# Kernel optimization log

Measured on AMD Instinct MI355X. Metric: run time of the kernel, lower is better.

## Reference

```python
import jax, jax.numpy as jnp
import numpy as np

B = 4
C = 128           # input channels
H = W = 512       # image size
P = 16            # patch size
GH = GW = 32      # token grid (H//P, W//P)
N = GH * GW       # num patches = 1024
PATCH_DIM = C * P * P  # 32768
DIM = 512         # embed dim
MLP = 256         # ffn hidden
DH = 64           # dim per head
HEADS = (2, 4, 8) # per-layer head counts
NUM_REL = (2 * GH - 1) * (2 * GW - 1)  # 3969


def _rel_index():
    # faithful to the torch buffer construction (meshgrid default 'ij')
    coords = np.stack(np.meshgrid(np.arange(GH), np.arange(GW), indexing='ij')).reshape(2, -1)
    rc = (coords[:, :, None] - coords[:, None, :]).transpose(1, 2, 0)  # [N,N,2]
    rc[..., 0] += GH - 1
    rc[..., 1] += GW - 1
    rc[..., 0] *= 2 * GH - 1
    return jnp.asarray(rc.sum(-1))  # [N,N] int

REL_IDX = _rel_index()


def _ln(x, s, b):
    m = x.mean(-1, keepdims=True)
    v = x.var(-1, keepdims=True)
    return (x - m) / jnp.sqrt(v + 1e-5) * s + b


def setup_inputs() -> dict:
    key = jax.random.key(0)
    ks = iter(jax.random.split(key, 40))
    def rn(shape, scale=0.02):
        return jax.random.normal(next(ks), shape, jnp.float32) * scale
    inp = {"img": jax.random.normal(next(ks), (B, C, H, W), jnp.float32)}
    inp["patch_w"] = rn((PATCH_DIM, DIM))
    inp["patch_b"] = jnp.zeros((DIM,), jnp.float32)
    inp["pos_emb"] = rn((1, N, DIM), 1.0)
    inp["ln1_s"] = jnp.ones((3, DIM), jnp.float32)
    inp["ln1_b"] = jnp.zeros((3, DIM), jnp.float32)
    inp["ln2_s"] = jnp.ones((3, DIM), jnp.float32)
    inp["ln2_b"] = jnp.zeros((3, DIM), jnp.float32)
    for l, h in enumerate(HEADS):
        inner = DH * h
        inp[f"qkv_w{l}"] = rn((DIM, 3 * inner))
        inp[f"out_w{l}"] = rn((inner, DIM))
        inp[f"out_b{l}"] = jnp.zeros((DIM,), jnp.float32)
        inp[f"bias{l}"] = rn((NUM_REL, h))
    inp["ff_w1"] = rn((3, DIM, MLP))
    inp["ff_b1"] = jnp.zeros((3, MLP), jnp.float32)
    inp["ff_w2"] = rn((3, MLP, DIM))
    inp["ff_b2"] = jnp.zeros((3, DIM), jnp.float32)
    return inp


def reference(img, patch_w, patch_b, pos_emb, ln1_s, ln1_b, ln2_s, ln2_b,
              qkv_w0, qkv_w1, qkv_w2, out_w0, out_w1, out_w2,
              out_b0, out_b1, out_b2, bias0, bias1, bias2,
              ff_w1, ff_b1, ff_w2, ff_b2):
    b = img.shape[0]
    # Rearrange 'b c (h p1) (w p2) -> b (h w) (p1 p2 c)'
    x = img.reshape(b, C, GH, P, GW, P).transpose(0, 2, 4, 3, 5, 1).reshape(b, N, PATCH_DIM)
    x = x @ patch_w + patch_b + pos_emb

    qkv_ws = (qkv_w0, qkv_w1, qkv_w2)
    out_ws = (out_w0, out_w1, out_w2)
    out_bs = (out_b0, out_b1, out_b2)
    tables = (bias0, bias1, bias2)

    for l, h in enumerate(HEADS):
        # attention with relative position bias
        xn = _ln(x, ln1_s[l], ln1_b[l])
        qkv = xn @ qkv_ws[l]                                  # [b, N, 3*h*DH]
        q, k, v = jnp.split(qkv, 3, axis=-1)
        q = q.reshape(b, N, h, DH).transpose(0, 2, 1, 3)      # bhnd
        k = k.reshape(b, N, h, DH).transpose(0, 2, 1, 3)
        v = v.reshape(b, N, h, DH).transpose(0, 2, 1, 3)
        dots = jnp.einsum('bhnd,bhmd->bhnm', q, k) * (DH ** -0.5)
        rel = tables[l][REL_IDX].transpose(2, 0, 1)           # [h, N, N]
        attn = jax.nn.softmax(dots + rel[None], axis=-1)
        o = jnp.einsum('bhnm,bhmd->bhnd', attn, v)
        o = o.transpose(0, 2, 1, 3).reshape(b, N, h * DH)
        x = o @ out_ws[l] + out_bs[l] + x
        # feed-forward
        xn = _ln(x, ln2_s[l], ln2_b[l])
        hmid = jax.nn.gelu(xn @ ff_w1[l] + ff_b1[l], approximate=False)
        x = hmid @ ff_w2[l] + ff_b2[l] + x

    return x.transpose(0, 2, 1).reshape(b, DIM, GH, GW)
```

## Files before the change

kernel.cpp:

```cpp
#include <hip/hip_runtime.h>

typedef unsigned short u16;
typedef __bf16 bf16x8 __attribute__((ext_vector_type(8)));
typedef float f32x4 __attribute__((ext_vector_type(4)));

#define AS1 __attribute__((address_space(1)))
#define AS3 __attribute__((address_space(3)))
#define MFMA(a,b,c) __builtin_amdgcn_mfma_f32_16x16x32_bf16(a,b,c,0,0,0)

__device__ __forceinline__ u16 f2bf(float f) {
    union { float f; unsigned u; } x; x.f = f;
    unsigned r = x.u + 0x7fffu + ((x.u >> 16) & 1u);
    return (u16)(r >> 16);
}

__global__ void k_patch_wT(const float* __restrict__ w, u16* __restrict__ o)
{
    __shared__ u16 T[256*33];
    int c = blockIdx.x, n0 = blockIdx.y*32;
    int t = threadIdx.x;
    int rr = t >> 5, cc = t & 31;
    #pragma unroll
    for (int i = 0; i < 32; ++i) {
        int r = i*8 + rr;
        int k = (r >> 4)*2048 + (r & 15)*128 + c;
        T[r*33 + cc] = f2bf(w[(size_t)k*512 + n0 + cc]);
    }
    __syncthreads();
    #pragma unroll
    for (int i = 0; i < 4; ++i) {
        int j  = i*8 + (t >> 5);
        int ch = t & 31;
        union { u16 u[8]; uint4 v; } pk;
        #pragma unroll
        for (int q = 0; q < 8; ++q) pk.u[q] = T[(ch*8+q)*33 + j];
        *(uint4*)(o + (size_t)(n0 + j)*32768 + c*256 + ch*8) = pk.v;
    }
}

__global__ void k_init_x(float* __restrict__ x, const float* __restrict__ pb, const float* __restrict__ pe)
{
    int i4 = blockIdx.x*256 + threadIdx.x;
    size_t base = (size_t)i4*4;
    float4 a = *(const float4*)(pb + (base & 511));
    float4 b = *(const float4*)(pe + (base & 524287));
    float4 r = make_float4(a.x+b.x, a.y+b.y, a.z+b.z, a.w+b.w);
    *(float4*)(x + base) = r;
}

struct TXJob { const float* in; u16* out; int K, N, tiles; };
struct TXArgs { TXJob j[12]; };

__global__ void k_wT_all(TXArgs a)
{
    __shared__ float T[32*33];
    int bid = blockIdx.x;
    int ji = 0;
    while (bid >= a.j[ji].tiles) { bid -= a.j[ji].tiles; ++ji; }
    const float* __restrict__ in = a.j[ji].in;
    u16* __restrict__ o = a.j[ji].out;
    const int K = a.j[ji].K, N = a.j[ji].N;
    const int tn = N >> 5;
    const int kt = (bid / tn) * 32, nt = (bid % tn) * 32;
    int t = threadIdx.x, r = t >> 5, c = t & 31;
    #pragma unroll
    for (int i = 0; i < 4; ++i)
        T[(r + i*8)*33 + c] = in[(size_t)(kt + r + i*8)*N + nt + c];
    __syncthreads();
    #pragma unroll
    for (int i = 0; i < 4; ++i)
        o[(size_t)(nt + r + i*8)*K + kt + c] = f2bf(T[c*33 + r + i*8]);
}

__global__ __launch_bounds__(1024) void k_patch_gemm(
    const float* __restrict__ img, const u16* __restrict__ Bt, float* __restrict__ Cf)
{
    __shared__ alignas(16) u16 As[2*128*64];
    __shared__ alignas(16) u16 Bs[2*512*64];
    const int t = threadIdx.x;
    const int bid = blockIdx.x;
    const int z = bid & 7;
    const int tile = bid >> 3;
    const int b = tile >> 3, gh0 = (tile & 7)*4;
    const int m0 = tile*128;
    const int wave = t >> 6, lane = t & 63;
    const int r16 = lane & 15, g = lane >> 4;
    const int wm = (wave >> 3)*64, wn = (wave & 7)*64;

    const int arow = t >> 6;
    const int ghl = arow >> 2, p1l = arow & 3;
    const int aw = (t & 63)*8;
    const int tok = ghl*32 + (aw >> 4);
    unsigned abyte = (unsigned)(tok*128 + p1l*32 + (aw & 15)*2);
    abyte ^= (unsigned)((tok & 7) << 4);
    const float* imgb = img + (size_t)b*128*262144
                      + (size_t)((gh0 + ghl)*16 + p1l)*512 + aw;
    const int brow = t >> 3;
    const int bchunk = (t & 7) ^ (brow & 7);
    const u16* Bb = Bt + (size_t)brow*32768 + (size_t)z*4096 + bchunk*8;
    u16* Bsd = Bs + t*8;

    f32x4 acc[4][4];
    const f32x4 zz = {0.f,0.f,0.f,0.f};
    #pragma unroll
    for (int im = 0; im < 4; ++im)
        #pragma unroll
        for (int in_ = 0; in_ < 4; ++in_) acc[im][in_] = zz;

#define ALOAD(KC) do {                                                               \
    const int c_ = z*16 + ((KC) >> 2);                                               \
    const float* s_ = imgb + (size_t)c_*262144 + ((KC) & 3)*2048;                    \
    e0 = *(const float4*)s_;  e1 = *(const float4*)(s_ + 4); } while(0)
#define AWRITE(BUF) do {                                                             \
    union { u16 u[8]; uint4 v; } pk_;                                                \
    pk_.u[0]=f2bf(e0.x); pk_.u[1]=f2bf(e0.y); pk_.u[2]=f2bf(e0.z); pk_.u[3]=f2bf(e0.w); \
    pk_.u[4]=f2bf(e1.x); pk_.u[5]=f2bf(e1.y); pk_.u[6]=f2bf(e1.z); pk_.u[7]=f2bf(e1.w); \
    *(uint4*)((char*)As + (BUF)*16384 + abyte) = pk_.v; } while(0)
#define BSTAGE(KC, BUF) do { _Pragma("unroll")                                       \
    for (int i_ = 0; i_ < 4; ++i_)                                                   \
        __builtin_amdgcn_global_load_lds((AS1 void*)(Bb + (size_t)i_*128*32768 + (KC)*64), \
                                         (AS3 void*)(Bsd + (BUF)*32768 + i_*8192), 16, 0, 0); } while(0)
#define WAITVM(N) asm volatile("s_waitcnt vmcnt(" #N ")" ::: "memory")
#define WAITLG   asm volatile("s_waitcnt lgkmcnt(0)" ::: "memory")

    float4 e0, e1;
    ALOAD(0);
    BSTAGE(0, 0);
    WAITVM(4);
    AWRITE(0);
    ALOAD(1);
    BSTAGE(1, 1);
    WAITLG;
    WAITVM(6);
    __builtin_amdgcn_s_barrier();
    __builtin_amdgcn_sched_barrier(0);

    int cur = 0;
    for (int kc = 0; kc < 64; ++kc) {
        const char* Asb = (const char*)As + cur*16384;
        const char* Bsb = (const char*)Bs + cur*65536;
        #pragma unroll
        for (int kk = 0; kk < 64; kk += 32) {
            bf16x8 af[4], bfr[4];
            #pragma unroll
            for (int im = 0; im < 4; ++im) {
                unsigned off = ((unsigned)((wm + im*16 + r16)*128 + kk*2 + g*16))
                             ^ (unsigned)((r16 & 7) << 4);
                af[im] = *(const bf16x8*)(Asb + off);
            }
            #pragma unroll
            for (int in_ = 0; in_ < 4; ++in_) {
                unsigned off = ((unsigned)((wn + in_*16 + r16)*128 + kk*2 + g*16))
                             ^ (unsigned)((r16 & 7) << 4);
                bfr[in_] = *(const bf16x8*)(Bsb + off);
            }
            #pragma unroll
            for (int im = 0; im < 4; ++im)
                #pragma unroll
                for (int in_ = 0; in_ < 4; ++in_)
                    acc[im][in_] = MFMA(af[im], bfr[in_], acc[im][in_]);
        }
        if (kc < 63) {
            WAITVM(4);
            AWRITE(cur ^ 1);
        }
        WAITLG;
        __builtin_amdgcn_s_barrier();
        if (kc < 62) {
            ALOAD(kc + 2);
            BSTAGE(kc + 2, cur);
            WAITVM(6);
        } else {
            WAITVM(0);
        }
        __builtin_amdgcn_sched_barrier(0);
        cur ^= 1;
    }
#undef ALOAD
#undef AWRITE
#undef BSTAGE
#undef WAITVM
#undef WAITLG
    #pragma unroll
    for (int im = 0; im < 4; ++im) {
        int row = m0 + wm + im*16 + g*4;
        #pragma unroll
        for (int in_ = 0; in_ < 4; ++in_) {
            int col = wn + in_*16 + r16;
            #pragma unroll
            for (int r = 0; r < 4; ++r)
                __hip_atomic_fetch_add(&Cf[(size_t)(row + r)*512 + col], acc[im][in_][r],
                                       __ATOMIC_RELAXED, __HIP_MEMORY_SCOPE_AGENT);
        }
    }
}

__global__ void k_ln(const float* __restrict__ x, const float* __restrict__ sc,
                     const float* __restrict__ bi, u16* __restrict__ o)
{
    int row = blockIdx.x, lane = threadIdx.x;
    const float* xr = x + (size_t)row*512 + lane*8;
    float4 v0 = *(const float4*)xr;
    float4 v1 = *(const float4*)(xr + 4);
    float vv[8] = {v0.x,v0.y,v0.z,v0.w,v1.x,v1.y,v1.z,v1.w};
    float sum = 0.f, sq = 0.f;
    #pragma unroll
    for (int i = 0; i < 8; ++i) { sum += vv[i]; sq += vv[i]*vv[i]; }
    #pragma unroll
    for (int m = 1; m < 64; m <<= 1) { sum += __shfl_xor(sum, m, 64); sq += __shfl_xor(sq, m, 64); }
    float mean = sum * (1.f/512.f);
    float var  = sq  * (1.f/512.f) - mean*mean;
    float rstd = rsqrtf(var + 1e-5f);
    int d = lane*8;
    union { u16 u[8]; uint4 v; } pk;
    #pragma unroll
    for (int i = 0; i < 8; ++i) pk.u[i] = f2bf((vv[i]-mean)*rstd*sc[d+i] + bi[d+i]);
    *(uint4*)(o + (size_t)row*512 + d) = pk.v;
}

template<int EPI, int KB>
__global__ __launch_bounds__(256) void k_gemm(
    const u16* __restrict__ A, int lda,
    const u16* __restrict__ Bt, int ldb,
    float* __restrict__ Cf, u16* __restrict__ Cb, int ldc,
    const float* __restrict__ bias)
{
    __shared__ alignas(16) u16 As[128*64];
    __shared__ alignas(16) u16 Bs[128*64];
    const int t = threadIdx.x;
    const int m0 = blockIdx.x*128, n0 = blockIdx.y*128;
    const int wave = t >> 6, lane = t & 63;
    const int wm = (wave >> 1)*64, wn = (wave & 1)*64;
    const int r16 = lane & 15, g = lane >> 4;
    const u16* Ab = A + (size_t)(m0 + (t>>3))*lda + (t&7)*8;
    const u16* Bb = Bt + (size_t)(n0 + (t>>3))*ldb + (t&7)*8;
    u16* Asd = As + t*8;
    u16* Bsd = Bs + t*8;
    f32x4 acc[4][4];
    const f32x4 z4 = {0.f,0.f,0.f,0.f};
    #pragma unroll
    for (int im = 0; im < 4; ++im)
        #pragma unroll
        for (int in_ = 0; in_ < 4; ++in_) acc[im][in_] = z4;

    #pragma unroll
    for (int k = 0; k < KB; k += 64) {
        #pragma unroll
        for (int i = 0; i < 4; ++i) {
            __builtin_amdgcn_global_load_lds((AS1 void*)(Ab + (size_t)i*32*lda + k), (AS3 void*)(Asd + i*2048), 16, 0, 0);
            __builtin_amdgcn_global_load_lds((AS1 void*)(Bb + (size_t)i*32*ldb + k), (AS3 void*)(Bsd + i*2048), 16, 0, 0);
        }
        __syncthreads();
        #pragma unroll
        for (int kk = 0; kk < 64; kk += 32) {
            bf16x8 af[4], bfr[4];
            #pragma unroll
            for (int im = 0; im < 4; ++im)
                af[im] = *(const bf16x8*)(As + (wm + im*16 + r16)*64 + kk + g*8);
            #pragma unroll
            for (int in_ = 0; in_ < 4; ++in_)
                bfr[in_] = *(const bf16x8*)(Bs + (wn + in_*16 + r16)*64 + kk + g*8);
            #pragma unroll
            for (int im = 0; im < 4; ++im)
                #pragma unroll
                for (int in_ = 0; in_ < 4; ++in_)
                    acc[im][in_] = MFMA(af[im], bfr[in_], acc[im][in_]);
        }
        __syncthreads();
    }
    #pragma unroll
    for (int im = 0; im < 4; ++im) {
        int row = m0 + wm + im*16 + g*4;
        #pragma unroll
        for (int in_ = 0; in_ < 4; ++in_) {
            int col = n0 + wn + in_*16 + r16;
            #pragma unroll
            for (int r = 0; r < 4; ++r) {
                float v = acc[im][in_][r];
                size_t idx = (size_t)(row + r)*ldc + col;
                if constexpr (EPI == 1) {
                    Cb[idx] = f2bf(v);
                } else if constexpr (EPI == 2) {
                    float xv = v + bias[col];
                    Cb[idx] = f2bf(0.5f*xv*(1.f + erff(xv*0.70710678118654752f)));
                } else {
                    Cf[idx] += v + bias[col];
                }
            }
        }
    }
}

__global__ __launch_bounds__(256) void k_attn(
    const u16* __restrict__ qkv, const float* __restrict__ bt,
    u16* __restrict__ o, int H)
{
    const int LD = 80;
    __shared__ alignas(16) u16 Qs[64*80], Ks[64*80], Vs[64*80];
    __shared__ alignas(16) u16 Ps[4][16*80];
    const int inner = H*64, s3 = 3*inner;
    const int qt = blockIdx.x, head = blockIdx.y, b = blockIdx.z;
    const int t = threadIdx.x, wave = t >> 6, lane = t & 63;
    const int r16 = lane & 15, g = lane >> 4;
    const int q0 = qt*64;
    const size_t tokbase = (size_t)b*1024;
    const int hoff = head*64;

    #pragma unroll
    for (int it = 0; it < 2; ++it) {
        int flat = it*256 + t, r = flat >> 3, d0 = (flat & 7)*8;
        uint4 v = *(const uint4*)(qkv + (tokbase + q0 + r)*s3 + hoff + d0);
        *(uint4*)(Qs + r*LD + d0) = v;
    }
    __syncthreads();
    bf16x8 aQ0 = *(const bf16x8*)(Qs + (wave*16 + r16)*LD + g*8);
    bf16x8 aQ1 = *(const bf16x8*)(Qs + (wave*16 + r16)*LD + 32 + g*8);

    float m_[4], l_[4];
    f32x4 O[4];
    const f32x4 z4 = {0.f,0.f,0.f,0.f};
    #pragma unroll
    for (int r = 0; r < 4; ++r) { m_[r] = -1e30f; l_[r] = 0.f; O[r] = z4; }
    const int qg_base = q0 + wave*16 + g*4;

    for (int kt = 0; kt < 16; ++kt) {
        const int key0 = kt*64;
        #pragma unroll
        for (int it = 0; it < 2; ++it) {
            int flat = it*256 + t, r = flat >> 3, d0 = (flat & 7)*8;
            uint4 v = *(const uint4*)(qkv + (tokbase + key0 + r)*s3 + inner + hoff + d0);
            *(uint4*)(Ks + r*LD + d0) = v;
        }
        #pragma unroll
        for (int it = 0; it < 2; ++it) {
            int flat = it*256 + t, key = flat & 63, d0 = (flat >> 6)*8;
            uint4 v = *(const uint4*)(qkv + (tokbase + key0 + key)*s3 + 2*inner + hoff + d0);
            const u16* pv = (const u16*)&v;
            #pragma unroll
            for (int i = 0; i < 8; ++i) Vs[(d0+i)*LD + key] = pv[i];
        }
        __syncthreads();

        float Sv[4][4];
        #pragma unroll
        for (int kb = 0; kb < 4; ++kb) {
            bf16x8 k0f = *(const bf16x8*)(Ks + (kb*16 + r16)*LD + g*8);
            bf16x8 k1f = *(const bf16x8*)(Ks + (kb*16 + r16)*LD + 32 + g*8);
            f32x4 S = z4;
            S = MFMA(aQ0, k0f, S);
            S = MFMA(aQ1, k1f, S);
            int keyg = key0 + kb*16 + r16;
            int kgh = keyg >> 5, kgw = keyg & 31;
            #pragma unroll
            for (int r = 0; r < 4; ++r) {
                int qg = qg_base + r;
                int rel = ((qg >> 5) - kgh + 31)*63 + ((qg & 31) - kgw + 31);
                Sv[kb][r] = S[r]*0.125f + bt[rel*H + head];
            }
        }
        float mx[4], al[4], ps[4];
        #pragma unroll
        for (int r = 0; r < 4; ++r)
            mx[r] = fmaxf(fmaxf(Sv[0][r], Sv[1][r]), fmaxf(Sv[2][r], Sv[3][r]));
        #pragma unroll
        for (int msk = 1; msk < 16; msk <<= 1)
            #pragma unroll
            for (int r = 0; r < 4; ++r) mx[r] = fmaxf(mx[r], __shfl_xor(mx[r], msk, 64));
        #pragma unroll
        for (int r = 0; r < 4; ++r) {
            float nm = fmaxf(m_[r], mx[r]);
            al[r] = __expf(m_[r] - nm);
            m_[r] = nm;
            ps[r] = 0.f;
        }
        #pragma unroll
        for (int kb = 0; kb < 4; ++kb)
            #pragma unroll
            for (int r = 0; r < 4; ++r) {
                float p = __expf(Sv[kb][r] - m_[r]);
                Sv[kb][r] = p;
                ps[r] += p;
            }
        #pragma unroll
        for (int msk = 1; msk < 16; msk <<= 1)
            #pragma unroll
            for (int r = 0; r < 4; ++r) ps[r] += __shfl_xor(ps[r], msk, 64);
        #pragma unroll
        for (int r = 0; r < 4; ++r) l_[r] = l_[r]*al[r] + ps[r];
        #pragma unroll
        for (int kb = 0; kb < 4; ++kb)
            #pragma unroll
            for (int r = 0; r < 4; ++r)
                Ps[wave][(g*4 + r)*LD + kb*16 + r16] = f2bf(Sv[kb][r]);
        #pragma unroll
        for (int dt = 0; dt < 4; ++dt)
            #pragma unroll
            for (int r = 0; r < 4; ++r) O[dt][r] = O[dt][r]*al[r];
        __syncthreads();
        bf16x8 aP0 = *(const bf16x8*)(Ps[wave] + r16*LD + g*8);
        bf16x8 aP1 = *(const bf16x8*)(Ps[wave] + r16*LD + 32 + g*8);
        #pragma unroll
        for (int dt = 0; dt < 4; ++dt) {
            bf16x8 v0 = *(const bf16x8*)(Vs + (dt*16 + r16)*LD + g*8);
            bf16x8 v1 = *(const bf16x8*)(Vs + (dt*16 + r16)*LD + 32 + g*8);
            O[dt] = MFMA(aP0, v0, O[dt]);
            O[dt] = MFMA(aP1, v1, O[dt]);
        }
        __syncthreads();
    }
    #pragma unroll
    for (int dt = 0; dt < 4; ++dt)
        #pragma unroll
        for (int r = 0; r < 4; ++r) {
            int token = q0 + wave*16 + g*4 + r;
            o[(tokbase + token)*inner + hoff + dt*16 + r16] = f2bf(O[dt][r] / l_[r]);
        }
}

__global__ void k_out_transpose(const float* __restrict__ x, float* __restrict__ o)
{
    __shared__ float T[32*33];
    int d0 = blockIdx.x*32, n0 = blockIdx.y*32, b = blockIdx.z;
    int t = threadIdx.x, r = t >> 5, c = t & 31;
    #pragma unroll
    for (int i = 0; i < 4; ++i)
        T[(r+i*8)*33 + c] = x[((size_t)b*1024 + n0 + r + i*8)*512 + d0 + c];
    __syncthreads();
    #pragma unroll
    for (int i = 0; i < 4; ++i)
        o[((size_t)b*512 + d0 + r + i*8)*1024 + n0 + c] = T[c*33 + (r+i*8)];
}

extern "C" void kernel_launch(void* const* d_in, const int* in_sizes, int n_in,
                              void* d_out, int out_size, void* d_ws, size_t ws_size,
                              hipStream_t stream)
{
    (void)in_sizes; (void)n_in; (void)out_size; (void)ws_size;
    const float* img     = (const float*)d_in[0];
    const float* patch_w = (const float*)d_in[1];
    const float* patch_b = (const float*)d_in[2];
    const float* pos_emb = (const float*)d_in[3];
    const float* ln1_s   = (const float*)d_in[4];
    const float* ln1_b   = (const float*)d_in[5];
    const float* ln2_s   = (const float*)d_in[6];
    const float* ln2_b   = (const float*)d_in[7];
    const float* qkv_w[3] = {(const float*)d_in[8],  (const float*)d_in[12], (const float*)d_in[16]};
    const float* out_w[3] = {(const float*)d_in[9],  (const float*)d_in[13], (const float*)d_in[17]};
    const float* out_b[3] = {(const float*)d_in[10], (const float*)d_in[14], (const float*)d_in[18]};
    const float* biasT[3] = {(const float*)d_in[11], (const float*)d_in[15], (const float*)d_in[19]};
    const float* ff_w1 = (const float*)d_in[20];
    const float* ff_b1 = (const float*)d_in[21];
    const float* ff_w2 = (const float*)d_in[22];
    const float* ff_b2 = (const float*)d_in[23];
    float* out = (float*)d_out;

    const int HS[3] = {2, 4, 8};

    char* ws = (char*)d_ws;
    size_t off = 0;
    auto alloc = [&](size_t bytes) -> void* {
        void* p = ws + off; off += (bytes + 255) & ~(size_t)255; return p;
    };
    u16*   pwT  = (u16*)  alloc(512ull*32768*2);
    float* x    = (float*)alloc(4096ull*512*4);
    u16*   xn   = (u16*)  alloc(4096ull*512*2);
    u16*   qkv  = (u16*)  alloc(4096ull*1536*2);
    u16*   ob   = (u16*)  alloc(4096ull*512*2);
    u16*   mid  = (u16*)  alloc(4096ull*256*2);
    u16*   qkvT = (u16*)  alloc(2688ull*512*2);
    u16*   outT = (u16*)  alloc(512ull*896*2);
    u16*   f1T  = (u16*)  alloc(3ull*256*512*2);
    u16*   f2T  = (u16*)  alloc(3ull*512*256*2);

    u16* qkvT_l[3] = { qkvT, qkvT + 384ull*512, qkvT + (384ull+768)*512 };
    u16* outT_l[3] = { outT, outT + 512ull*128, outT + 512ull*(128+256) };
    u16* f1T_l[3]  = { f1T,  f1T  + 256ull*512, f1T  + 2ull*256*512 };
    u16* f2T_l[3]  = { f2T,  f2T  + 512ull*256, f2T  + 2ull*512*256 };

    k_patch_wT<<<dim3(128,16), 256, 0, stream>>>(patch_w, pwT);
    k_init_x<<<2048, 256, 0, stream>>>(x, patch_b, pos_emb);

    TXArgs tx;
    int tj = 0, total_tiles = 0;
    auto add_job = [&](const float* in, u16* o, int K, int N) {
        tx.j[tj] = TXJob{in, o, K, N, (K/32)*(N/32)};
        total_tiles += tx.j[tj].tiles; ++tj;
    };
    for (int l = 0; l < 3; ++l) add_job(qkv_w[l], qkvT_l[l], 512, 3*64*HS[l]);
    for (int l = 0; l < 3; ++l) add_job(out_w[l], outT_l[l], 64*HS[l], 512);
    for (int l = 0; l < 3; ++l) add_job(ff_w1 + (size_t)l*512*256, f1T_l[l], 512, 256);
    for (int l = 0; l < 3; ++l) add_job(ff_w2 + (size_t)l*256*512, f2T_l[l], 256, 512);
    k_wT_all<<<total_tiles, 256, 0, stream>>>(tx);

    k_patch_gemm<<<256, 1024, 0, stream>>>(img, pwT, x);

    for (int l = 0; l < 3; ++l) {
        int h = HS[l], inner = 64*h, n3 = 3*inner;

        k_ln<<<4096, 64, 0, stream>>>(x, ln1_s + l*512, ln1_b + l*512, xn);
        k_gemm<1,512><<<dim3(32, n3/128), 256, 0, stream>>>(xn, 512, qkvT_l[l], 512,
                                                            nullptr, qkv, n3, nullptr);
        k_attn<<<dim3(16, h, 4), 256, 0, stream>>>(qkv, biasT[l], ob, h);
        if (l == 0)
            k_gemm<3,128><<<dim3(32, 4), 256, 0, stream>>>(ob, inner, outT_l[l], inner,
                                                           x, nullptr, 512, out_b[l]);
        else if (l == 1)
            k_gemm<3,256><<<dim3(32, 4), 256, 0, stream>>>(ob, inner, outT_l[l], inner,
                                                           x, nullptr, 512, out_b[l]);
        else
            k_gemm<3,512><<<dim3(32, 4), 256, 0, stream>>>(ob, inner, outT_l[l], inner,
                                                           x, nullptr, 512, out_b[l]);
        k_ln<<<4096, 64, 0, stream>>>(x, ln2_s + l*512, ln2_b + l*512, xn);
        k_gemm<2,512><<<dim3(32, 2), 256, 0, stream>>>(xn, 512, f1T_l[l], 512,
                                                       nullptr, mid, 256, ff_b1 + l*256);
        k_gemm<3,256><<<dim3(32, 4), 256, 0, stream>>>(mid, 256, f2T_l[l], 256,
                                                       x, nullptr, 512, ff_b2 + l*512);
    }
    k_out_transpose<<<dim3(16, 32, 4), 256, 0, stream>>>(x, out);
}
```

Baseline: 735.2 us.

## Fuse LayerNorm into preceding GEMMs via last-block ticket and merge prologue kernels

Removes the standalone LayerNorm launches. Each GEMM that updates the residual x now bumps a per-row-tile atomic ticket, and the last block to finish a row tile computes LayerNorm for those 128 rows and writes bf16 xn. The three setup kernels (patch-weight transpose, x init, weight transposes) are merged into one prologue launch, which also zeroes the tickets. This saves launch overhead and a separate pass over x, but adds thread fences and atomics, and puts the LayerNorm work on a single serial block per tile.

```diff
diff --git a/kernel.cpp b/kernel.cpp
--- a/kernel.cpp
+++ b/kernel.cpp
@@ -14,66 +14,68 @@
     return (u16)(r >> 16);
 }
 
-__global__ void k_patch_wT(const float* __restrict__ w, u16* __restrict__ o)
-{
-    __shared__ u16 T[256*33];
-    int c = blockIdx.x, n0 = blockIdx.y*32;
-    int t = threadIdx.x;
-    int rr = t >> 5, cc = t & 31;
-    #pragma unroll
-    for (int i = 0; i < 32; ++i) {
-        int r = i*8 + rr;
-        int k = (r >> 4)*2048 + (r & 15)*128 + c;
-        T[r*33 + cc] = f2bf(w[(size_t)k*512 + n0 + cc]);
-    }
-    __syncthreads();
-    #pragma unroll
-    for (int i = 0; i < 4; ++i) {
-        int j  = i*8 + (t >> 5);
-        int ch = t & 31;
-        union { u16 u[8]; uint4 v; } pk;
-        #pragma unroll
-        for (int q = 0; q < 8; ++q) pk.u[q] = T[(ch*8+q)*33 + j];
-        *(uint4*)(o + (size_t)(n0 + j)*32768 + c*256 + ch*8) = pk.v;
-    }
-}
-
-__global__ void k_init_x(float* __restrict__ x, const float* __restrict__ pb, const float* __restrict__ pe)
-{
-    int i4 = blockIdx.x*256 + threadIdx.x;
-    size_t base = (size_t)i4*4;
-    float4 a = *(const float4*)(pb + (base & 511));
-    float4 b = *(const float4*)(pe + (base & 524287));
-    float4 r = make_float4(a.x+b.x, a.y+b.y, a.z+b.z, a.w+b.w);
-    *(float4*)(x + base) = r;
-}
-
 struct TXJob { const float* in; u16* out; int K, N, tiles; };
 struct TXArgs { TXJob j[12]; };
 
-__global__ void k_wT_all(TXArgs a)
+__global__ __launch_bounds__(256) void k_prologue(
+    const float* __restrict__ patch_w, u16* __restrict__ pwT,
+    const float* __restrict__ pb, const float* __restrict__ pe, float* __restrict__ x,
+    TXArgs a, int* __restrict__ tickets)
 {
-    __shared__ float T[32*33];
-    int bid = blockIdx.x;
-    int ji = 0;
-    while (bid >= a.j[ji].tiles) { bid -= a.j[ji].tiles; ++ji; }
-    const float* __restrict__ in = a.j[ji].in;
-    u16* __restrict__ o = a.j[ji].out;
-    const int K = a.j[ji].K, N = a.j[ji].N;
-    const int tn = N >> 5;
-    const int kt = (bid / tn) * 32, nt = (bid % tn) * 32;
-    int t = threadIdx.x, r = t >> 5, c = t & 31;
-    #pragma unroll
-    for (int i = 0; i < 4; ++i)
-        T[(r + i*8)*33 + c] = in[(size_t)(kt + r + i*8)*N + nt + c];
-    __syncthreads();
-    #pragma unroll
-    for (int i = 0; i < 4; ++i)
-        o[(size_t)(nt + r + i*8)*K + kt + c] = f2bf(T[c*33 + r + i*8]);
+    __shared__ alignas(16) char smem[256*33*2];
+    const int bid = blockIdx.x, t = threadIdx.x;
+    if (bid == 0 && t < 224) tickets[t] = 0;
+    if (bid < 2048) {
+        u16* T = (u16*)smem;
+        int c = bid & 127, n0 = (bid >> 7)*32;
+        int rr = t >> 5, cc = t & 31;
+        #pragma unroll
+        for (int i = 0; i < 32; ++i) {
+            int r = i*8 + rr;
+            int k = (r >> 4)*2048 + (r & 15)*128 + c;
+            T[r*33 + cc] = f2bf(patch_w[(size_t)k*512 + n0 + cc]);
+        }
+        __syncthreads();
+        #pragma unroll
+        for (int i = 0; i < 4; ++i) {
+            int j  = i*8 + (t >> 5);
+            int ch = t & 31;
+            union { u16 u[8]; uint4 v; } pk;
+            #pragma unroll
+            for (int q = 0; q < 8; ++q) pk.u[q] = T[(ch*8+q)*33 + j];
+            *(uint4*)(pwT + (size_t)(n0 + j)*32768 + c*256 + ch*8) = pk.v;
+        }
+    } else if (bid < 4096) {
+        int i4 = (bid - 2048)*256 + t;
+        size_t base = (size_t)i4*4;
+        float4 av = *(const float4*)(pb + (base & 511));
+        float4 bv = *(const float4*)(pe + (base & 524287));
+        *(float4*)(x + base) = make_float4(av.x+bv.x, av.y+bv.y, av.z+bv.z, av.w+bv.w);
+    } else {
+        float* T = (float*)smem;
+        int tb = bid - 4096;
+        int ji = 0;
+        while (tb >= a.j[ji].tiles) { tb -= a.j[ji].tiles; ++ji; }
+        const float* __restrict__ in = a.j[ji].in;
+        u16* __restrict__ o = a.j[ji].out;
+        const int K = a.j[ji].K, N = a.j[ji].N;
+        const int tn = N >> 5;
+        const int kt = (tb / tn) * 32, nt = (tb % tn) * 32;
+        int r = t >> 5, c = t & 31;
+        #pragma unroll
+        for (int i = 0; i < 4; ++i)
+            T[(r + i*8)*33 + c] = in[(size_t)(kt + r + i*8)*N + nt + c];
+        __syncthreads();
+        #pragma unroll
+        for (int i = 0; i < 4; ++i)
+            o[(size_t)(nt + r + i*8)*K + kt + c] = f2bf(T[c*33 + r + i*8]);
+    }
 }
 
 __global__ __launch_bounds__(1024) void k_patch_gemm(
-    const float* __restrict__ img, const u16* __restrict__ Bt, float* __restrict__ Cf)
+    const float* __restrict__ img, const u16* __restrict__ Bt, float* __restrict__ Cf,
+    const float* __restrict__ lnsc, const float* __restrict__ lnbi,
+    u16* __restrict__ lnout, int* __restrict__ ticket)
 {
     __shared__ alignas(16) u16 As[2*128*64];
     __shared__ alignas(16) u16 Bs[2*512*64];
@@ -193,29 +195,38 @@
                                        __ATOMIC_RELAXED, __HIP_MEMORY_SCOPE_AGENT);
         }
     }
-}
-
-__global__ void k_ln(const float* __restrict__ x, const float* __restrict__ sc,
-                     const float* __restrict__ bi, u16* __restrict__ o)
-{
-    int row = blockIdx.x, lane = threadIdx.x;
-    const float* xr = x + (size_t)row*512 + lane*8;
-    float4 v0 = *(const float4*)xr;
-    float4 v1 = *(const float4*)(xr + 4);
-    float vv[8] = {v0.x,v0.y,v0.z,v0.w,v1.x,v1.y,v1.z,v1.w};
-    float sum = 0.f, sq = 0.f;
-    #pragma unroll
-    for (int i = 0; i < 8; ++i) { sum += vv[i]; sq += vv[i]*vv[i]; }
-    #pragma unroll
-    for (int m = 1; m < 64; m <<= 1) { sum += __shfl_xor(sum, m, 64); sq += __shfl_xor(sq, m, 64); }
-    float mean = sum * (1.f/512.f);
-    float var  = sq  * (1.f/512.f) - mean*mean;
-    float rstd = rsqrtf(var + 1e-5f);
-    int d = lane*8;
-    union { u16 u[8]; uint4 v; } pk;
-    #pragma unroll
-    for (int i = 0; i < 8; ++i) pk.u[i] = f2bf((vv[i]-mean)*rstd*sc[d+i] + bi[d+i]);
-    *(uint4*)(o + (size_t)row*512 + d) = pk.v;
+    __threadfence();
+    __syncthreads();
+    int* winp = (int*)As;
+    if (t == 0) {
+        int prev = __hip_atomic_fetch_add(&ticket[tile], 1, __ATOMIC_ACQ_REL, __HIP_MEMORY_SCOPE_AGENT);
+        *winp = (prev == 7);
+    }
+    __syncthreads();
+    if (*winp) {
+        __threadfence();
+        #pragma unroll
+        for (int i = 0; i < 8; ++i) {
+            int row = m0 + i*16 + wave;
+            const float* xr = Cf + (size_t)row*512 + lane*8;
+            float4 v0 = *(const float4*)xr;
+            float4 v1 = *(const float4*)(xr + 4);
+            float vv[8] = {v0.x,v0.y,v0.z,v0.w,v1.x,v1.y,v1.z,v1.w};
+            float sum = 0.f, sq = 0.f;
+            #pragma unroll
+            for (int q = 0; q < 8; ++q) { sum += vv[q]; sq += vv[q]*vv[q]; }
+            #pragma unroll
+            for (int m = 1; m < 64; m <<= 1) { sum += __shfl_xor(sum, m, 64); sq += __shfl_xor(sq, m, 64); }
+            float mean = sum * (1.f/512.f);
+            float var  = sq  * (1.f/512.f) - mean*mean;
+            float rstd = rsqrtf(var + 1e-5f);
+            int d = lane*8;
+            union { u16 u[8]; uint4 v; } pk;
+            #pragma unroll
+            for (int q = 0; q < 8; ++q) pk.u[q] = f2bf((vv[q]-mean)*rstd*lnsc[d+q] + lnbi[d+q]);
+            *(uint4*)(lnout + (size_t)row*512 + d) = pk.v;
+        }
+    }
 }
 
 template<int EPI, int KB>
@@ -223,7 +234,9 @@
     const u16* __restrict__ A, int lda,
     const u16* __restrict__ Bt, int ldb,
     float* __restrict__ Cf, u16* __restrict__ Cb, int ldc,
-    const float* __restrict__ bias)
+    const float* __restrict__ bias,
+    const float* __restrict__ lnsc, const float* __restrict__ lnbi,
+    u16* __restrict__ lnout, int* __restrict__ ticket)
 {
     __shared__ alignas(16) u16 As[128*64];
     __shared__ alignas(16) u16 Bs[128*64];
@@ -286,6 +299,40 @@
                 } else {
                     Cf[idx] += v + bias[col];
                 }
+            }
+        }
+    }
+    if constexpr (EPI == 4) {
+        __threadfence();
+        __syncthreads();
+        int* winp = (int*)As;
+        if (t == 0) {
+            int prev = __hip_atomic_fetch_add(&ticket[blockIdx.x], 1, __ATOMIC_ACQ_REL, __HIP_MEMORY_SCOPE_AGENT);
+            *winp = (prev == 3);
+        }
+        __syncthreads();
+        if (*winp) {
+            __threadfence();
+            #pragma unroll
+            for (int i = 0; i < 32; ++i) {
+                int row = m0 + i*4 + wave;
+                const float* xr = Cf + (size_t)row*512 + lane*8;
+                float4 v0 = *(const float4*)xr;
+                float4 v1 = *(const float4*)(xr + 4);
+                float vv[8] = {v0.x,v0.y,v0.z,v0.w,v1.x,v1.y,v1.z,v1.w};
+                float sum = 0.f, sq = 0.f;
+                #pragma unroll
+                for (int q = 0; q < 8; ++q) { sum += vv[q]; sq += vv[q]*vv[q]; }
+                #pragma unroll
+                for (int m = 1; m < 64; m <<= 1) { sum += __shfl_xor(sum, m, 64); sq += __shfl_xor(sq, m, 64); }
+                float mean = sum * (1.f/512.f);
+                float var  = sq  * (1.f/512.f) - mean*mean;
+                float rstd = rsqrtf(var + 1e-5f);
+                int d = lane*8;
+                union { u16 u[8]; uint4 v; } pk;
+                #pragma unroll
+                for (int q = 0; q < 8; ++q) pk.u[q] = f2bf((vv[q]-mean)*rstd*lnsc[d+q] + lnbi[d+q]);
+                *(uint4*)(lnout + (size_t)row*512 + d) = pk.v;
             }
         }
     }
@@ -471,14 +518,12 @@
     u16*   outT = (u16*)  alloc(512ull*896*2);
     u16*   f1T  = (u16*)  alloc(3ull*256*512*2);
     u16*   f2T  = (u16*)  alloc(3ull*512*256*2);
+    int*   tk   = (int*)  alloc(224*4);
 
     u16* qkvT_l[3] = { qkvT, qkvT + 384ull*512, qkvT + (384ull+768)*512 };
     u16* outT_l[3] = { outT, outT + 512ull*128, outT + 512ull*(128+256) };
     u16* f1T_l[3]  = { f1T,  f1T  + 256ull*512, f1T  + 2ull*256*512 };
     u16* f2T_l[3]  = { f2T,  f2T  + 512ull*256, f2T  + 2ull*512*256 };
-
-    k_patch_wT<<<dim3(128,16), 256, 0, stream>>>(patch_w, pwT);
-    k_init_x<<<2048, 256, 0, stream>>>(x, patch_b, pos_emb);
 
     TXArgs tx;
     int tj = 0, total_tiles = 0;
@@ -490,31 +535,36 @@
     for (int l = 0; l < 3; ++l) add_job(out_w[l], outT_l[l], 64*HS[l], 512);
     for (int l = 0; l < 3; ++l) add_job(ff_w1 + (size_t)l*512*256, f1T_l[l], 512, 256);
     for (int l = 0; l < 3; ++l) add_job(ff_w2 + (size_t)l*256*512, f2T_l[l], 256, 512);
-    k_wT_all<<<total_tiles, 256, 0, stream>>>(tx);
-
-    k_patch_gemm<<<256, 1024, 0, stream>>>(img, pwT, x);
+    k_prologue<<<4096 + total_tiles, 256, 0, stream>>>(patch_w, pwT, patch_b, pos_emb, x, tx, tk);
+
+    k_patch_gemm<<<256, 1024, 0, stream>>>(img, pwT, x, ln1_s, ln1_b, xn, tk);
 
     for (int l = 0; l < 3; ++l) {
         int h = HS[l], inner = 64*h, n3 = 3*inner;
-
-        k_ln<<<4096, 64, 0, stream>>>(x, ln1_s + l*512, ln1_b + l*512, xn);
+        int* tk_out = tk + 32*(1 + 2*l);
+        int* tk_ff2 = tk + 32*(2 + 2*l);
+
         k_gemm<1,512><<<dim3(32, n3/128), 256, 0, stream>>>(xn, 512, qkvT_l[l], 512,
-                                                            nullptr, qkv, n3, nullptr);
+                nullptr, qkv, n3, nullptr, nullptr, nullptr, nullptr, nullptr);
         k_attn<<<dim3(16, h, 4), 256, 0, stream>>>(qkv, biasT[l], ob, h);
         if (l == 0)
-            k_gemm<3,128><<<dim3(32, 4), 256, 0, stream>>>(ob, inner, outT_l[l], inner,
-                                                           x, nullptr, 512, out_b[l]);
+            k_gemm<4,128><<<dim3(32, 4), 256, 0, stream>>>(ob, inner, outT_l[l], inner,
+                    x, nullptr, 512, out_b[l], ln2_s + l*512, ln2_b + l*512, xn, tk_out);
         else if (l == 1)
-            k_gemm<3,256><<<dim3(32, 4), 256, 0, stream>>>(ob, inner, outT_l[l], inner,
-                                                           x, nullptr, 512, out_b[l]);
+            k_gemm<4,256><<<dim3(32, 4), 256, 0, stream>>>(ob, inner, outT_l[l], inner,
+                    x, nullptr, 512, out_b[l], ln2_s + l*512, ln2_b + l*512, xn, tk_out);
         else
-            k_gemm<3,512><<<dim3(32, 4), 256, 0, stream>>>(ob, inner, outT_l[l], inner,
-                                                           x, nullptr, 512, out_b[l]);
-        k_ln<<<4096, 64, 0, stream>>>(x, ln2_s + l*512, ln2_b + l*512, xn);
+            k_gemm<4,512><<<dim3(32, 4), 256, 0, stream>>>(ob, inner, outT_l[l], inner,
+                    x, nullptr, 512, out_b[l], ln2_s + l*512, ln2_b + l*512, xn, tk_out);
         k_gemm<2,512><<<dim3(32, 2), 256, 0, stream>>>(xn, 512, f1T_l[l], 512,
-                                                       nullptr, mid, 256, ff_b1 + l*256);
-        k_gemm<3,256><<<dim3(32, 4), 256, 0, stream>>>(mid, 256, f2T_l[l], 256,
-                                                       x, nullptr, 512, ff_b2 + l*512);
+                nullptr, mid, 256, ff_b1 + l*256, nullptr, nullptr, nullptr, nullptr);
+        if (l < 2)
+            k_gemm<4,256><<<dim3(32, 4), 256, 0, stream>>>(mid, 256, f2T_l[l], 256,
+                    x, nullptr, 512, ff_b2 + l*512,
+                    ln1_s + (l+1)*512, ln1_b + (l+1)*512, xn, tk_ff2);
+        else
+            k_gemm<3,256><<<dim3(32, 4), 256, 0, stream>>>(mid, 256, f2T_l[l], 256,
+                    x, nullptr, 512, ff_b2 + l*512, nullptr, nullptr, nullptr, nullptr);
     }
     k_out_transpose<<<dim3(16, 32, 4), 256, 0, stream>>>(x, out);
 }
```

New measurement: 1.080 ms. 46.9% more time.
